# Optimization experiments

Measured on AMD Instinct MI355X. Metric: run time of the kernel, lower is better.

Reference implementation:

```python
import jax, jax.numpy as jnp
import numpy as np

VOCAB, EMBED = 100000, 128
B, QLEN, DLEN = 1024, 32, 256
KERNEL_NUM, SIGMA, EXACT_SIGMA = 11, 0.1, 0.001
EPS = 1e-8  # torch F.cosine_similarity eps


def _kernel_mus(n):
    l_mu = [1.0]
    if n == 1:
        return l_mu
    bin_size = 2.0 / (n - 1)
    l_mu.append(1 - bin_size / 2)
    for i in range(1, n - 1):
        l_mu.append(round(l_mu[i] - bin_size, 5))
    return list(reversed(l_mu))


def _kernel_sigmas(n, sigma, exact_sigma):
    l_sigma = [exact_sigma]
    if n == 1:
        return l_sigma
    l_sigma += [sigma] * (n - 1)
    return list(reversed(l_sigma))


MUS = jnp.asarray(np.array(_kernel_mus(KERNEL_NUM), dtype=np.float32))      # [K]
SIGMAS = jnp.asarray(np.array(_kernel_sigmas(KERNEL_NUM, SIGMA, EXACT_SIGMA), dtype=np.float32))  # [K]


def setup_inputs() -> dict:
    key = jax.random.key(0)
    k = jax.random.split(key, 7)
    return {
        "emb": jax.random.normal(k[0], (VOCAB, EMBED), dtype=jnp.float32),
        "mlp_w": jax.random.normal(k[1], (1, KERNEL_NUM), dtype=jnp.float32) * 0.3,
        "mlp_b": jax.random.normal(k[2], (1,), dtype=jnp.float32) * 0.1,
        "query1": jax.random.randint(k[3], (B, QLEN), 0, VOCAB, dtype=jnp.int32).astype(jnp.int64),
        "doc1": jax.random.randint(k[4], (B, DLEN), 0, VOCAB, dtype=jnp.int32).astype(jnp.int64),
        "query2": jax.random.randint(k[5], (B, QLEN), 0, VOCAB, dtype=jnp.int32).astype(jnp.int64),
        "doc2": jax.random.randint(k[6], (B, DLEN), 0, VOCAB, dtype=jnp.int32).astype(jnp.int64),
    }


def _predict(emb, mlp_w, mlp_b, query, doc):
    qe = emb[query]                               # [B,Q,E]
    de = emb[doc]                                 # [B,D,E]
    qn = jnp.linalg.norm(qe, axis=-1)             # [B,Q]
    dn = jnp.linalg.norm(de, axis=-1)             # [B,D]
    dots = jnp.einsum("bqe,bde->bqd", qe, de)    # [B,Q,D]
    sim = dots / jnp.maximum(qn[:, :, None] * dn[:, None, :], EPS)
    # multi-Gaussian soft histogram: exp(-(sim-mu)^2/(2 sigma^2)), sum over doc,
    # log1p, sum over query  -> [B,K]
    z = (sim[..., None] - MUS) / SIGMAS           # [B,Q,D,K]
    K = jnp.exp(-0.5 * z * z)
    pooled = jnp.log1p(K.sum(axis=2)).sum(axis=1)  # [B,K]
    return pooled @ mlp_w.T + mlp_b               # [B,1]


def reference(emb, mlp_w, mlp_b, query1, doc1, query2, doc2):
    logits_1 = _predict(emb, mlp_w, mlp_b, query1, doc1)
    logits_2 = _predict(emb, mlp_w, mlp_b, query2, doc2)
    return jax.nn.sigmoid(logits_1 - logits_2)    # [B,1]
```

## Files before the change

kernel.cpp:

```cpp
#include <hip/hip_runtime.h>
#include <math.h>
#include <stdint.h>

#define VOCAB 100000
#define NB    1024
#define QLEN  32
#define DLEN  256
#define EMBED 128
#define KNUM  11

typedef __attribute__((ext_vector_type(8))) short bf16x8;
typedef __attribute__((ext_vector_type(4))) float f32x4;

#define HALF_L2E 0.7213475204444817f
#define TWO_L2E  2.8853900817779268f
#define EM4      0.018315638888734179f

#define SSTR  68
#define SHALF (16 * SSTR)

__global__ __launch_bounds__(256)
void cvt_table(const float* __restrict__ emb, ushort* __restrict__ ebf)
{
    const int row = blockIdx.x * 8 + (threadIdx.x >> 5);
    const int l32 = threadIdx.x & 31;
    const float4 v = *((const float4*)(emb + (size_t)row * EMBED) + l32);
    union { float f; unsigned u; } x0, x1, x2, x3;
    x0.f = v.x; x1.f = v.y; x2.f = v.z; x3.f = v.w;
    const unsigned r0 = x0.u + 0x8000u, r1 = x1.u + 0x8000u;
    const unsigned r2 = x2.u + 0x8000u, r3 = x3.u + 0x8000u;
    uint2 packed;
    packed.x = (r0 >> 16) | (r1 & 0xFFFF0000u);
    packed.y = (r2 >> 16) | (r3 & 0xFFFF0000u);
    *((uint2*)(ebf + (size_t)row * EMBED) + l32) = packed;
}

__device__ __forceinline__ void chain4(const f32x4 sv, float (&ksum)[KNUM])
{
    #pragma unroll
    for (int e = 0; e < 4; ++e) {
        const float s  = sv[e];
        const float z  = fmaf(s, 10.f, -1.f);
        const float e0 = exp2f(-HALF_L2E * (z * z));
        float ru = exp2f(fmaf(z,  TWO_L2E, -TWO_L2E));
        float rd = exp2f(fmaf(z, -TWO_L2E, -TWO_L2E));
        ksum[5] += e0;
        float tt = e0;
        tt *= ru; ksum[6] += tt; ru *= EM4;
        tt *= ru; ksum[7] += tt; ru *= EM4;
        tt *= ru; ksum[8] += tt; ru *= EM4;
        tt *= ru; ksum[9] += tt;
        tt = e0;
        tt *= rd; ksum[4] += tt; rd *= EM4;
        tt *= rd; ksum[3] += tt; rd *= EM4;
        tt *= rd; ksum[2] += tt; rd *= EM4;
        tt *= rd; ksum[1] += tt; rd *= EM4;
        tt *= rd; ksum[0] += tt;
        ksum[10] += (s > 0.995f) ? 1.f : 0.f;
    }
}

__device__ __forceinline__ void pool_half(float* __restrict__ wtile,
                                          const f32x4* __restrict__ a,
                                          const float* __restrict__ riq,
                                          const float* __restrict__ idn,
                                          float (*__restrict__ stot)[12],
                                          int mtbase, int l15, int quad)
{
    #pragma unroll
    for (int nt = 0; nt < 4; ++nt)
        #pragma unroll
        for (int r = 0; r < 4; ++r)
            wtile[(quad * 4 + r) * SSTR + nt * 16 + l15] = a[nt][r] * riq[r] * idn[nt];

    const float* rp = wtile + l15 * SSTR + quad * 16;
    float ksum[KNUM];
    #pragma unroll
    for (int k = 0; k < KNUM; ++k) ksum[k] = 0.f;
    #pragma unroll
    for (int i = 0; i < 4; ++i)
        chain4(*(const f32x4*)(rp + 4 * i), ksum);
    #pragma unroll
    for (int k = 0; k < KNUM; ++k) {
        ksum[k] += __shfl_xor(ksum[k], 16);
        ksum[k] += __shfl_xor(ksum[k], 32);
    }
    if (quad == 0) {
        #pragma unroll
        for (int k = 0; k < KNUM; ++k)
            atomicAdd(&stot[mtbase + l15][k], ksum[k]);
    }
}

__device__ __forceinline__ float sumsq8(const bf16x8 v, float acc)
{
    #pragma unroll
    for (int e = 0; e < 8; ++e) {
        union { unsigned u; float f; } g;
        g.u = ((unsigned)(unsigned short)v[e]) << 16;
        acc = fmaf(g.f, g.f, acc);
    }
    return acc;
}

__global__ __launch_bounds__(256, 4)
void knrm_pair7(const ushort* __restrict__ ebf,
                const float* __restrict__ mlp_w,
                const int* __restrict__ q1, const int* __restrict__ d1,
                const int* __restrict__ q2, const int* __restrict__ d2,
                float* __restrict__ logits)
{
    const int b    = blockIdx.x;
    const int pair = blockIdx.y;
    const int t    = threadIdx.x;
    const int w    = t >> 6;
    const int l    = t & 63;
    const int l15  = l & 15;
    const int quad = l >> 4;

    const int* __restrict__ qry = (pair == 0 ? q1 : q2) + b * QLEN;
    const int* __restrict__ doc = (pair == 0 ? d1 : d2) + b * DLEN;

    __shared__ __align__(16) float s_buf[4][SHALF];
    __shared__ __align__(16) uint4 s_q[2 * 256];
    __shared__ float s_tot[QLEN][12];

    #define SWZ(r, s) (((r) << 4) | (((s) ^ (r)) & 15))

    uint4* wbuf = (uint4*)&s_buf[w][0];

    #pragma unroll
    for (int i = 0; i < 2; ++i) {
        const int row = w * 8 + i * 4 + quad;
        const int id  = qry[row];
        const uint4 v = *(const uint4*)(ebf + (size_t)id * EMBED + l15 * 8);
        s_q[(row >> 4) * 256 + SWZ(row & 15, l15)] = v;
    }
    #pragma unroll
    for (int i = t; i < QLEN * 12; i += 256) ((float*)s_tot)[i] = 0.f;
    __syncthreads();

    bf16x8 a0[4], a1[4];
    float qn0 = 0.f, qn1 = 0.f;
    #pragma unroll
    for (int kk = 0; kk < 4; ++kk) {
        const int s = quad + 4 * kk;
        a0[kk] = *(const bf16x8*)&s_q[      SWZ(l15, s)];
        a1[kk] = *(const bf16x8*)&s_q[256 + SWZ(l15, s)];
        qn0 = sumsq8(a0[kk], qn0);
        qn1 = sumsq8(a1[kk], qn1);
    }
    qn0 += __shfl_xor(qn0, 16); qn0 += __shfl_xor(qn0, 32);
    qn1 += __shfl_xor(qn1, 16); qn1 += __shfl_xor(qn1, 32);
    float riq[2][4];
    #pragma unroll
    for (int r = 0; r < 4; ++r) {
        riq[0][r] = __builtin_amdgcn_rsqf(__shfl(qn0, quad * 4 + r));
        riq[1][r] = __builtin_amdgcn_rsqf(__shfl(qn1, quad * 4 + r));
    }

    f32x4 acc[2][4];
    #pragma unroll
    for (int mt = 0; mt < 2; ++mt)
        #pragma unroll
        for (int j = 0; j < 4; ++j)
            acc[mt][j] = (f32x4){0.f, 0.f, 0.f, 0.f};
    float idn[4];
    uint4 pf[4];

    #pragma unroll
    for (int i = 0; i < 4; ++i) {
        const int id = doc[w * 64 + 4 * i + quad];
        pf[i] = *(const uint4*)(ebf + (size_t)id * EMBED + l15 * 8);
    }

    #pragma unroll
    for (int j = 0; j < 4; ++j) {
        #pragma unroll
        for (int i = 0; i < 4; ++i)
            wbuf[SWZ(4 * i + quad, l15)] = pf[i];
        if (j < 3) {
            #pragma unroll
            for (int i = 0; i < 4; ++i) {
                const int id = doc[w * 64 + (j + 1) * 16 + 4 * i + quad];
                pf[i] = *(const uint4*)(ebf + (size_t)id * EMBED + l15 * 8);
            }
        }
        asm volatile("s_waitcnt lgkmcnt(0)" ::: "memory");
        __builtin_amdgcn_sched_barrier(0);

        bf16x8 bb[4];
        float dn = 0.f;
        #pragma unroll
        for (int kk = 0; kk < 4; ++kk) {
            bb[kk] = *(const bf16x8*)&wbuf[SWZ(l15, quad + 4 * kk)];
            dn = sumsq8(bb[kk], dn);
        }
        dn += __shfl_xor(dn, 16); dn += __shfl_xor(dn, 32);
        idn[j] = __builtin_amdgcn_rsqf(dn);

        #pragma unroll
        for (int kk = 0; kk < 4; ++kk) {
            acc[0][j] = __builtin_amdgcn_mfma_f32_16x16x32_bf16(a0[kk], bb[kk], acc[0][j], 0, 0, 0);
            acc[1][j] = __builtin_amdgcn_mfma_f32_16x16x32_bf16(a1[kk], bb[kk], acc[1][j], 0, 0, 0);
        }
        __builtin_amdgcn_sched_barrier(0);
    }

    float* wtile = &s_buf[w][0];
    pool_half(wtile, acc[0], riq[0], idn, s_tot, 0,  l15, quad);
    pool_half(wtile, acc[1], riq[1], idn, s_tot, 16, l15, quad);
    __syncthreads();

    if (t < QLEN) {
        float c = 0.f;
        #pragma unroll
        for (int k = 0; k < KNUM; ++k) c += mlp_w[k] * log1pf(s_tot[t][k]);
        #pragma unroll
        for (int mm = 1; mm < 32; mm <<= 1) c += __shfl_xor(c, mm);
        if (t == 0) logits[pair * NB + b] = c;
    }
    #undef SWZ
}

__device__ __forceinline__ bf16x8 cvt8(const float* p, float& nacc)
{
    uint4 a = *((const uint4*)p);
    uint4 b = *((const uint4*)(p + 4));
    unsigned u[8] = {a.x, a.y, a.z, a.w, b.x, b.y, b.z, b.w};
    bf16x8 r;
    #pragma unroll
    for (int i = 0; i < 8; ++i) {
        const unsigned q = u[i] + 0x8000u;
        r[i] = (short)(q >> 16);
        union { unsigned uu; float ff; } g; g.uu = q & 0xFFFF0000u;
        nacc = fmaf(g.ff, g.ff, nacc);
    }
    return r;
}

__global__ __launch_bounds__(256, 4)
void knrm_pair_fb(const float* __restrict__ emb,
                  const float* __restrict__ mlp_w,
                  const int* __restrict__ q1, const int* __restrict__ d1,
                  const int* __restrict__ q2, const int* __restrict__ d2,
                  float* __restrict__ logits)
{
    const int b    = blockIdx.x;
    const int pair = blockIdx.y;
    const int t    = threadIdx.x;
    const int w    = t >> 6;
    const int l15  = t & 15;
    const int quad = (t & 63) >> 4;

    const int* __restrict__ qry = (pair == 0 ? q1 : q2) + b * QLEN;
    const int* __restrict__ doc = (pair == 0 ? d1 : d2) + b * DLEN;

    __shared__ __align__(16) float s_sim[4 * SHALF];
    __shared__ float s_tot[QLEN][12];

    #pragma unroll
    for (int i = t; i < QLEN * 12; i += 256) ((float*)s_tot)[i] = 0.f;
    __syncthreads();

    const int qid0 = qry[l15], qid1 = qry[l15 + 16];
    int did[4];
    #pragma unroll
    for (int nt = 0; nt < 4; ++nt) did[nt] = doc[(w * 4 + nt) * 16 + l15];

    f32x4 acc[2][4];
    #pragma unroll
    for (int mt = 0; mt < 2; ++mt)
        #pragma unroll
        for (int nt = 0; nt < 4; ++nt)
            acc[mt][nt] = (f32x4){0.f, 0.f, 0.f, 0.f};

    float idn[4], riq[2][4];
    float* wtile = s_sim + w * SHALF;

    {
        float qn2[2] = {0.f, 0.f}, dn2[4] = {0.f, 0.f, 0.f, 0.f};
        const float* qp0 = emb + (size_t)qid0 * EMBED + quad * 8;
        const float* qp1 = emb + (size_t)qid1 * EMBED + quad * 8;
        #pragma unroll
        for (int kk = 0; kk < 4; ++kk) {
            const bf16x8 a0 = cvt8(qp0 + kk * 32, qn2[0]);
            const bf16x8 a1 = cvt8(qp1 + kk * 32, qn2[1]);
            #pragma unroll
            for (int nt = 0; nt < 4; ++nt) {
                const bf16x8 bb = cvt8(emb + (size_t)did[nt] * EMBED + quad * 8 + kk * 32, dn2[nt]);
                acc[0][nt] = __builtin_amdgcn_mfma_f32_16x16x32_bf16(a0, bb, acc[0][nt], 0, 0, 0);
                acc[1][nt] = __builtin_amdgcn_mfma_f32_16x16x32_bf16(a1, bb, acc[1][nt], 0, 0, 0);
            }
        }
        #pragma unroll
        for (int i = 0; i < 2; ++i) {
            qn2[i] += __shfl_xor(qn2[i], 16);
            qn2[i] += __shfl_xor(qn2[i], 32);
        }
        #pragma unroll
        for (int nt = 0; nt < 4; ++nt) {
            dn2[nt] += __shfl_xor(dn2[nt], 16);
            dn2[nt] += __shfl_xor(dn2[nt], 32);
            idn[nt] = __builtin_amdgcn_rsqf(dn2[nt]);
        }
        #pragma unroll
        for (int r = 0; r < 4; ++r) {
            riq[0][r] = __builtin_amdgcn_rsqf(__shfl(qn2[0], quad * 4 + r));
            riq[1][r] = __builtin_amdgcn_rsqf(__shfl(qn2[1], quad * 4 + r));
        }
    }

    pool_half(wtile, acc[0], riq[0], idn, s_tot, 0,  l15, quad);
    pool_half(wtile, acc[1], riq[1], idn, s_tot, 16, l15, quad);
    __syncthreads();

    if (t < QLEN) {
        float c = 0.f;
        #pragma unroll
        for (int k = 0; k < KNUM; ++k) c += mlp_w[k] * log1pf(s_tot[t][k]);
        #pragma unroll
        for (int mm = 1; mm < 32; mm <<= 1) c += __shfl_xor(c, mm);
        if (t == 0) logits[pair * NB + b] = c;
    }
}

__global__ __launch_bounds__(256)
void knrm_combine(const float* __restrict__ logits, float* __restrict__ out)
{
    const int i = blockIdx.x * blockDim.x + threadIdx.x;
    if (i < NB) {
        const float d = logits[i] - logits[NB + i];
        out[i] = 1.f / (1.f + __expf(-d));
    }
}

extern "C" void kernel_launch(void* const* d_in, const int* in_sizes, int n_in,
                              void* d_out, int out_size, void* d_ws, size_t ws_size,
                              hipStream_t stream)
{
    const float* emb   = (const float*)d_in[0];
    const float* mlp_w = (const float*)d_in[1];
    const int* q1 = (const int*)d_in[3];
    const int* d1 = (const int*)d_in[4];
    const int* q2 = (const int*)d_in[5];
    const int* d2 = (const int*)d_in[6];

    float* out = (float*)d_out;

    const size_t need = 2 * NB * 4
                      + (size_t)VOCAB * EMBED * 2 + 256;
    if (ws_size >= need) {
        float*  logits = (float*)d_ws;
        ushort* ebf    = (ushort*)(logits + 2 * NB);
        cvt_table<<<VOCAB / 8, 256, 0, stream>>>(emb, ebf);
        knrm_pair7<<<dim3(NB, 2), 256, 0, stream>>>(ebf, mlp_w,
                                                    q1, d1, q2, d2, logits);
    } else {
        float* logits = (float*)d_ws;
        knrm_pair_fb<<<dim3(NB, 2), 256, 0, stream>>>(emb, mlp_w,
                                                      q1, d1, q2, d2, logits);
    }
    knrm_combine<<<(NB + 255) / 256, 256, 0, stream>>>((float*)d_ws, out);
}
```

Baseline: 147.1 us.

## Replace four-wave pairwise KNRM kernel with single-wave register-fed pipelined kernel

The main kernel now runs one 64-thread wave per (batch, pair) instead of four waves. Document embedding fragments are loaded straight from global memory into MFMA operand registers, with the next 32-document chunk prefetched while the current one is pooled. This removes LDS staging of doc rows, the __syncthreads barriers and the shared-memory atomics in the pooling step. In exchange, far fewer waves are resident to hide gather latency, and each wave processes the whole document serially.

```diff
diff --git a/kernel.cpp b/kernel.cpp
--- a/kernel.cpp
+++ b/kernel.cpp
@@ -18,6 +18,7 @@
 
 #define SSTR  68
 #define SHALF (16 * SSTR)
+#define SST9  36
 
 __global__ __launch_bounds__(256)
 void cvt_table(const float* __restrict__ emb, ushort* __restrict__ ebf)
@@ -60,6 +61,185 @@
     }
 }
 
+__device__ __forceinline__ float sumsq8(const bf16x8 v, float acc)
+{
+    #pragma unroll
+    for (int e = 0; e < 8; ++e) {
+        union { unsigned u; float f; } g;
+        g.u = ((unsigned)(unsigned short)v[e]) << 16;
+        acc = fmaf(g.f, g.f, acc);
+    }
+    return acc;
+}
+
+__device__ __forceinline__ void issue_frags9(const ushort* __restrict__ ebf,
+                                             int i0, int i1, int quad,
+                                             bf16x8 (&b0)[4], bf16x8 (&b1)[4])
+{
+    const ushort* p0 = ebf + (size_t)i0 * EMBED + quad * 8;
+    const ushort* p1 = ebf + (size_t)i1 * EMBED + quad * 8;
+    #pragma unroll
+    for (int kk = 0; kk < 4; ++kk) {
+        b0[kk] = *(const bf16x8*)(p0 + kk * 32);
+        b1[kk] = *(const bf16x8*)(p1 + kk * 32);
+    }
+}
+
+__device__ __forceinline__ void half_unit9(
+    const ushort* __restrict__ ebf, const int* __restrict__ doc,
+    int l15, int quad,
+    int u2, int& n2a, int& n2b,
+    int nxa, int nxb, bool hasNext,
+    bf16x8 (&b0)[4], bf16x8 (&b1)[4],
+    const bf16x8 (&a0)[4], const bf16x8 (&a1)[4],
+    const float (&riq)[2][4],
+    float* __restrict__ s_sim, float (*__restrict__ stot)[12])
+{
+    if (u2 >= 0) {
+        n2a = doc[u2 * 32 + l15];
+        n2b = doc[u2 * 32 + 16 + l15];
+    }
+
+    float dn0 = 0.f, dn1 = 0.f;
+    f32x4 p00 = {0.f,0.f,0.f,0.f}, p01 = p00, p10 = p00, p11 = p00;
+    #pragma unroll
+    for (int kk = 0; kk < 4; ++kk) {
+        p00 = __builtin_amdgcn_mfma_f32_16x16x32_bf16(a0[kk], b0[kk], p00, 0, 0, 0);
+        p10 = __builtin_amdgcn_mfma_f32_16x16x32_bf16(a1[kk], b0[kk], p10, 0, 0, 0);
+        dn0 = sumsq8(b0[kk], dn0);
+        p01 = __builtin_amdgcn_mfma_f32_16x16x32_bf16(a0[kk], b1[kk], p01, 0, 0, 0);
+        p11 = __builtin_amdgcn_mfma_f32_16x16x32_bf16(a1[kk], b1[kk], p11, 0, 0, 0);
+        dn1 = sumsq8(b1[kk], dn1);
+    }
+    dn0 += __shfl_xor(dn0, 16); dn0 += __shfl_xor(dn0, 32);
+    dn1 += __shfl_xor(dn1, 16); dn1 += __shfl_xor(dn1, 32);
+    const float idn0 = __builtin_amdgcn_rsqf(dn0);
+    const float idn1 = __builtin_amdgcn_rsqf(dn1);
+    #pragma unroll
+    for (int r = 0; r < 4; ++r) {
+        s_sim[(     quad * 4 + r) * SST9 +      l15] = p00[r] * riq[0][r] * idn0;
+        s_sim[(16 + quad * 4 + r) * SST9 +      l15] = p10[r] * riq[1][r] * idn0;
+        s_sim[(     quad * 4 + r) * SST9 + 16 + l15] = p01[r] * riq[0][r] * idn1;
+        s_sim[(16 + quad * 4 + r) * SST9 + 16 + l15] = p11[r] * riq[1][r] * idn1;
+    }
+
+    if (hasNext) issue_frags9(ebf, nxa, nxb, quad, b0, b1);
+
+    asm volatile("s_waitcnt lgkmcnt(0)" ::: "memory");
+    __builtin_amdgcn_sched_barrier(0);
+
+    #pragma unroll
+    for (int mt = 0; mt < 2; ++mt) {
+        const float* rp = s_sim + (mt * 16 + l15) * SST9 + quad * 8;
+        float ksum[KNUM];
+        #pragma unroll
+        for (int k = 0; k < KNUM; ++k) ksum[k] = 0.f;
+        chain4(*(const f32x4*)rp, ksum);
+        chain4(*(const f32x4*)(rp + 4), ksum);
+        #pragma unroll
+        for (int k = 0; k < KNUM; ++k) {
+            ksum[k] += __shfl_xor(ksum[k], 16);
+            ksum[k] += __shfl_xor(ksum[k], 32);
+        }
+        if (quad == 0) {
+            #pragma unroll
+            for (int k = 0; k < KNUM; ++k)
+                stot[mt * 16 + l15][k] += ksum[k];
+        }
+    }
+    __builtin_amdgcn_sched_barrier(0);
+}
+
+__global__ __launch_bounds__(64, 2)
+void knrm_pair9(const ushort* __restrict__ ebf,
+                const float* __restrict__ mlp_w,
+                const int* __restrict__ q1, const int* __restrict__ d1,
+                const int* __restrict__ q2, const int* __restrict__ d2,
+                float* __restrict__ logits)
+{
+    const int b    = blockIdx.x;
+    const int pair = blockIdx.y;
+    const int t    = threadIdx.x;
+    const int l15  = t & 15;
+    const int quad = t >> 4;
+
+    const int* __restrict__ qry = (pair == 0 ? q1 : q2) + b * QLEN;
+    const int* __restrict__ doc = (pair == 0 ? d1 : d2) + b * DLEN;
+
+    __shared__ __align__(16) float s_sim[32 * SST9];
+    __shared__ float s_tot[QLEN][12];
+
+    int ia0 = doc[l15],      ia1 = doc[16 + l15];
+    int ib0 = doc[32 + l15], ib1 = doc[48 + l15];
+    int ic0, ic1, dum0, dum1;
+
+    const int qid0 = qry[l15], qid1 = qry[l15 + 16];
+    bf16x8 a0[4], a1[4];
+    float qn0 = 0.f, qn1 = 0.f;
+    {
+        const ushort* p0 = ebf + (size_t)qid0 * EMBED + quad * 8;
+        const ushort* p1 = ebf + (size_t)qid1 * EMBED + quad * 8;
+        #pragma unroll
+        for (int kk = 0; kk < 4; ++kk) {
+            a0[kk] = *(const bf16x8*)(p0 + kk * 32);
+            a1[kk] = *(const bf16x8*)(p1 + kk * 32);
+            qn0 = sumsq8(a0[kk], qn0);
+            qn1 = sumsq8(a1[kk], qn1);
+        }
+    }
+    qn0 += __shfl_xor(qn0, 16); qn0 += __shfl_xor(qn0, 32);
+    qn1 += __shfl_xor(qn1, 16); qn1 += __shfl_xor(qn1, 32);
+    float riq[2][4];
+    #pragma unroll
+    for (int r = 0; r < 4; ++r) {
+        riq[0][r] = __builtin_amdgcn_rsqf(__shfl(qn0, quad * 4 + r));
+        riq[1][r] = __builtin_amdgcn_rsqf(__shfl(qn1, quad * 4 + r));
+    }
+
+    #pragma unroll
+    for (int i = t; i < QLEN * 12; i += 64) ((float*)s_tot)[i] = 0.f;
+
+    bf16x8 b0[4], b1[4];
+    issue_frags9(ebf, ia0, ia1, quad, b0, b1);
+
+    half_unit9(ebf, doc, l15, quad,  2, ic0, ic1, ib0, ib1, true,  b0, b1, a0, a1, riq, s_sim, s_tot);
+    half_unit9(ebf, doc, l15, quad,  3, ia0, ia1, ic0, ic1, true,  b0, b1, a0, a1, riq, s_sim, s_tot);
+    half_unit9(ebf, doc, l15, quad,  4, ib0, ib1, ia0, ia1, true,  b0, b1, a0, a1, riq, s_sim, s_tot);
+    half_unit9(ebf, doc, l15, quad,  5, ic0, ic1, ib0, ib1, true,  b0, b1, a0, a1, riq, s_sim, s_tot);
+    half_unit9(ebf, doc, l15, quad,  6, ia0, ia1, ic0, ic1, true,  b0, b1, a0, a1, riq, s_sim, s_tot);
+    half_unit9(ebf, doc, l15, quad,  7, ib0, ib1, ia0, ia1, true,  b0, b1, a0, a1, riq, s_sim, s_tot);
+    half_unit9(ebf, doc, l15, quad, -1, dum0, dum1, ib0, ib1, true,  b0, b1, a0, a1, riq, s_sim, s_tot);
+    half_unit9(ebf, doc, l15, quad, -1, dum0, dum1, 0, 0,     false, b0, b1, a0, a1, riq, s_sim, s_tot);
+
+    float wk[KNUM];
+    #pragma unroll
+    for (int k = 0; k < KNUM; ++k) wk[k] = mlp_w[k];
+    float c = 0.f;
+    if (t < QLEN) {
+        #pragma unroll
+        for (int k = 0; k < KNUM; ++k) c += wk[k] * log1pf(s_tot[t][k]);
+    }
+    #pragma unroll
+    for (int m = 1; m < 64; m <<= 1) c += __shfl_xor(c, m);
+    if (t == 0) logits[pair * NB + b] = c;
+}
+
+__device__ __forceinline__ bf16x8 cvt8(const float* p, float& nacc)
+{
+    uint4 a = *((const uint4*)p);
+    uint4 b = *((const uint4*)(p + 4));
+    unsigned u[8] = {a.x, a.y, a.z, a.w, b.x, b.y, b.z, b.w};
+    bf16x8 r;
+    #pragma unroll
+    for (int i = 0; i < 8; ++i) {
+        const unsigned q = u[i] + 0x8000u;
+        r[i] = (short)(q >> 16);
+        union { unsigned uu; float ff; } g; g.uu = q & 0xFFFF0000u;
+        nacc = fmaf(g.ff, g.ff, nacc);
+    }
+    return r;
+}
+
 __device__ __forceinline__ void pool_half(float* __restrict__ wtile,
                                           const f32x4* __restrict__ a,
                                           const float* __restrict__ riq,
@@ -90,153 +270,6 @@
         for (int k = 0; k < KNUM; ++k)
             atomicAdd(&stot[mtbase + l15][k], ksum[k]);
     }
-}
-
-__device__ __forceinline__ float sumsq8(const bf16x8 v, float acc)
-{
-    #pragma unroll
-    for (int e = 0; e < 8; ++e) {
-        union { unsigned u; float f; } g;
-        g.u = ((unsigned)(unsigned short)v[e]) << 16;
-        acc = fmaf(g.f, g.f, acc);
-    }
-    return acc;
-}
-
-__global__ __launch_bounds__(256, 4)
-void knrm_pair7(const ushort* __restrict__ ebf,
-                const float* __restrict__ mlp_w,
-                const int* __restrict__ q1, const int* __restrict__ d1,
-                const int* __restrict__ q2, const int* __restrict__ d2,
-                float* __restrict__ logits)
-{
-    const int b    = blockIdx.x;
-    const int pair = blockIdx.y;
-    const int t    = threadIdx.x;
-    const int w    = t >> 6;
-    const int l    = t & 63;
-    const int l15  = l & 15;
-    const int quad = l >> 4;
-
-    const int* __restrict__ qry = (pair == 0 ? q1 : q2) + b * QLEN;
-    const int* __restrict__ doc = (pair == 0 ? d1 : d2) + b * DLEN;
-
-    __shared__ __align__(16) float s_buf[4][SHALF];
-    __shared__ __align__(16) uint4 s_q[2 * 256];
-    __shared__ float s_tot[QLEN][12];
-
-    #define SWZ(r, s) (((r) << 4) | (((s) ^ (r)) & 15))
-
-    uint4* wbuf = (uint4*)&s_buf[w][0];
-
-    #pragma unroll
-    for (int i = 0; i < 2; ++i) {
-        const int row = w * 8 + i * 4 + quad;
-        const int id  = qry[row];
-        const uint4 v = *(const uint4*)(ebf + (size_t)id * EMBED + l15 * 8);
-        s_q[(row >> 4) * 256 + SWZ(row & 15, l15)] = v;
-    }
-    #pragma unroll
-    for (int i = t; i < QLEN * 12; i += 256) ((float*)s_tot)[i] = 0.f;
-    __syncthreads();
-
-    bf16x8 a0[4], a1[4];
-    float qn0 = 0.f, qn1 = 0.f;
-    #pragma unroll
-    for (int kk = 0; kk < 4; ++kk) {
-        const int s = quad + 4 * kk;
-        a0[kk] = *(const bf16x8*)&s_q[      SWZ(l15, s)];
-        a1[kk] = *(const bf16x8*)&s_q[256 + SWZ(l15, s)];
-        qn0 = sumsq8(a0[kk], qn0);
-        qn1 = sumsq8(a1[kk], qn1);
-    }
-    qn0 += __shfl_xor(qn0, 16); qn0 += __shfl_xor(qn0, 32);
-    qn1 += __shfl_xor(qn1, 16); qn1 += __shfl_xor(qn1, 32);
-    float riq[2][4];
-    #pragma unroll
-    for (int r = 0; r < 4; ++r) {
-        riq[0][r] = __builtin_amdgcn_rsqf(__shfl(qn0, quad * 4 + r));
-        riq[1][r] = __builtin_amdgcn_rsqf(__shfl(qn1, quad * 4 + r));
-    }
-
-    f32x4 acc[2][4];
-    #pragma unroll
-    for (int mt = 0; mt < 2; ++mt)
-        #pragma unroll
-        for (int j = 0; j < 4; ++j)
-            acc[mt][j] = (f32x4){0.f, 0.f, 0.f, 0.f};
-    float idn[4];
-    uint4 pf[4];
-
-    #pragma unroll
-    for (int i = 0; i < 4; ++i) {
-        const int id = doc[w * 64 + 4 * i + quad];
-        pf[i] = *(const uint4*)(ebf + (size_t)id * EMBED + l15 * 8);
-    }
-
-    #pragma unroll
-    for (int j = 0; j < 4; ++j) {
-        #pragma unroll
-        for (int i = 0; i < 4; ++i)
-            wbuf[SWZ(4 * i + quad, l15)] = pf[i];
-        if (j < 3) {
-            #pragma unroll
-            for (int i = 0; i < 4; ++i) {
-                const int id = doc[w * 64 + (j + 1) * 16 + 4 * i + quad];
-                pf[i] = *(const uint4*)(ebf + (size_t)id * EMBED + l15 * 8);
-            }
-        }
-        asm volatile("s_waitcnt lgkmcnt(0)" ::: "memory");
-        __builtin_amdgcn_sched_barrier(0);
-
-        bf16x8 bb[4];
-        float dn = 0.f;
-        #pragma unroll
-        for (int kk = 0; kk < 4; ++kk) {
-            bb[kk] = *(const bf16x8*)&wbuf[SWZ(l15, quad + 4 * kk)];
-            dn = sumsq8(bb[kk], dn);
-        }
-        dn += __shfl_xor(dn, 16); dn += __shfl_xor(dn, 32);
-        idn[j] = __builtin_amdgcn_rsqf(dn);
-
-        #pragma unroll
-        for (int kk = 0; kk < 4; ++kk) {
-            acc[0][j] = __builtin_amdgcn_mfma_f32_16x16x32_bf16(a0[kk], bb[kk], acc[0][j], 0, 0, 0);
-            acc[1][j] = __builtin_amdgcn_mfma_f32_16x16x32_bf16(a1[kk], bb[kk], acc[1][j], 0, 0, 0);
-        }
-        __builtin_amdgcn_sched_barrier(0);
-    }
-
-    float* wtile = &s_buf[w][0];
-    pool_half(wtile, acc[0], riq[0], idn, s_tot, 0,  l15, quad);
-    pool_half(wtile, acc[1], riq[1], idn, s_tot, 16, l15, quad);
-    __syncthreads();
-
-    if (t < QLEN) {
-        float c = 0.f;
-        #pragma unroll
-        for (int k = 0; k < KNUM; ++k) c += mlp_w[k] * log1pf(s_tot[t][k]);
-        #pragma unroll
-        for (int mm = 1; mm < 32; mm <<= 1) c += __shfl_xor(c, mm);
-        if (t == 0) logits[pair * NB + b] = c;
-    }
-    #undef SWZ
-}
-
-__device__ __forceinline__ bf16x8 cvt8(const float* p, float& nacc)
-{
-    uint4 a = *((const uint4*)p);
-    uint4 b = *((const uint4*)(p + 4));
-    unsigned u[8] = {a.x, a.y, a.z, a.w, b.x, b.y, b.z, b.w};
-    bf16x8 r;
-    #pragma unroll
-    for (int i = 0; i < 8; ++i) {
-        const unsigned q = u[i] + 0x8000u;
-        r[i] = (short)(q >> 16);
-        union { unsigned uu; float ff; } g; g.uu = q & 0xFFFF0000u;
-        nacc = fmaf(g.ff, g.ff, nacc);
-    }
-    return r;
 }
 
 __global__ __launch_bounds__(256, 4)
@@ -354,8 +387,8 @@
         float*  logits = (float*)d_ws;
         ushort* ebf    = (ushort*)(logits + 2 * NB);
         cvt_table<<<VOCAB / 8, 256, 0, stream>>>(emb, ebf);
-        knrm_pair7<<<dim3(NB, 2), 256, 0, stream>>>(ebf, mlp_w,
-                                                    q1, d1, q2, d2, logits);
+        knrm_pair9<<<dim3(NB, 2), 64, 0, stream>>>(ebf, mlp_w,
+                                                   q1, d1, q2, d2, logits);
     } else {
         float* logits = (float*)d_ws;
         knrm_pair_fb<<<dim3(NB, 2), 256, 0, stream>>>(emb, mlp_w,
```

Result: slower. 185.8 us (+26.3%).
